# Kernel tuning notes

Measured on AMD Instinct MI355X. Metric: run time of the kernel, lower is better.

The kernel has to match this reference:

```python
import jax, jax.numpy as jnp
from jax import lax
import numpy as np


def _gru(x, h, w_ih, w_hh, b_ih, b_hh):
    # torch.nn.GRUCell: gates ordered (r, z, n)
    gi = x @ w_ih.T + b_ih
    gh = h @ w_hh.T + b_hh
    ir, iz, inn = jnp.split(gi, 3, axis=-1)
    hr, hz, hn = jnp.split(gh, 3, axis=-1)
    r = jax.nn.sigmoid(ir + hr)
    z = jax.nn.sigmoid(iz + hz)
    n = jnp.tanh(inn + r * hn)
    return (1.0 - z) * n + z * h


def _conv(x, w, pad):
    return lax.conv_general_dilated(x, w, (1, 1), [(pad, pad), (pad, pad)],
                                    dimension_numbers=('NCHW', 'OIHW', 'NCHW'))


def _bn(x, g, b):
    # BatchNorm2d in training mode: batch stats over (N,H,W)
    mu = x.mean((0, 2, 3), keepdims=True)
    var = x.var((0, 2, 3), keepdims=True)
    return (x - mu) * lax.rsqrt(var + 1e-5) * g[None, :, None, None] + b[None, :, None, None]


def _forward(features, heights, proj_wtm, mask_outliers, map_height, map_width,
             w_ih, w_hh, b_ih, b_hh,
             c1_w, bn1_g, bn1_b, c2_w, bn2_g, bn2_b, c3_w, bn3_g, bn3_b,
             c4_w, bn4_g, bn4_b, c5_w, c5_b):
    T, C, H, W = features.shape
    M = map_height * map_width
    P = H * W
    mem_dim = w_hh.shape[1]
    # flat map indices per pixel per frame: map_width*y + x
    idx_all = (map_width * proj_wtm[..., 1] + proj_wtm[..., 0]).astype(jnp.int32).reshape(T, P)
    inliers = ~mask_outliers
    mh_all = jnp.where(inliers, heights + 1000.0, -jnp.inf).reshape(T, P)
    feats_flat = features.reshape(T, C, P)
    pix = jnp.arange(P, dtype=jnp.int32)

    def step(carry, frame):
        state, observed, hmap = carry
        feat, idx, mh = frame  # feat [C,P], idx [P] int, mh [P]
        new_hmap = hmap.at[idx].max(mh)                      # persistent scatter_max
        # winner pixel per map cell: a pixel that attains the new max this frame
        cand = jnp.where(mh == new_hmap[idx], pix, -1)
        winner = jnp.full((M,), -1, dtype=jnp.int32).at[idx].max(cand)
        updated = new_hmap > hmap                            # cells where this frame set a new max
        x = feat.T[jnp.maximum(winner, 0)]                   # [M, C] gathered features
        new_state = _gru(x, state, w_ih, w_hh, b_ih, b_hh)
        state = jnp.where(updated[:, None], new_state, state)
        return (state, observed | updated, new_hmap), None

    init = (jnp.zeros((M, mem_dim), features.dtype),
            jnp.zeros((M,), dtype=bool),
            jnp.zeros((M,), features.dtype))
    (state, observed, hmap), _ = lax.scan(step, init, (feats_flat, idx_all, mh_all))

    memory = state.reshape(map_height, map_width, mem_dim).transpose(2, 0, 1)[None]  # [1,D,mh,mw]
    x = jax.nn.relu(_bn(_conv(memory, c1_w, 3), bn1_g, bn1_b))
    x = jax.nn.relu(_bn(_conv(x, c2_w, 1), bn2_g, bn2_b))
    x = jax.nn.relu(_bn(_conv(x, c3_w, 1), bn3_g, bn3_b))
    x = jax.nn.relu(_bn(_conv(x, c4_w, 1), bn4_g, bn4_b))
    sem = _conv(x, c5_w, 0) + c5_b[None, :, None, None]
    return (sem[0],
            observed.reshape(map_height, map_width),
            hmap.reshape(map_height, map_width))


def setup_inputs() -> dict:
    key = jax.random.key(0)
    ks = jax.random.split(key, 24)
    T, C, H, W = 10, 64, 480, 640
    MH, MW, D, NC = 250, 250, 256, 20
    s = 0.02
    return {
        'features': jax.random.normal(ks[0], (T, C, H, W), jnp.float32),
        'proj_wtm': jax.random.randint(ks[1], (T, H, W, 2), 0, 250, jnp.int32),
        'mask_outliers': jax.random.bernoulli(ks[2], 0.3, (T, H, W)),
        'heights': jax.random.normal(ks[3], (T, H, W), jnp.float32),
        'map_height': MH,
        'map_width': MW,
        'w_ih': jax.random.uniform(ks[4], (3 * D, C), jnp.float32, -0.01, 0.01),
        'w_hh': jax.random.uniform(ks[5], (3 * D, D), jnp.float32, -0.01, 0.01),
        'b_ih': jax.random.uniform(ks[6], (3 * D,), jnp.float32, -0.01, 0.01),
        'b_hh': jnp.zeros((3 * D,), jnp.float32),
        'c1_w': jax.random.normal(ks[7], (128, D, 7, 7), jnp.float32) * s,
        'bn1_g': jnp.ones((128,), jnp.float32), 'bn1_b': jnp.full((128,), 1e-4, jnp.float32),
        'c2_w': jax.random.normal(ks[8], (64, 128, 3, 3), jnp.float32) * s,
        'bn2_g': jnp.ones((64,), jnp.float32), 'bn2_b': jnp.full((64,), 1e-4, jnp.float32),
        'c3_w': jax.random.normal(ks[9], (48, 64, 3, 3), jnp.float32) * s,
        'bn3_g': jnp.ones((48,), jnp.float32), 'bn3_b': jnp.full((48,), 1e-4, jnp.float32),
        'c4_w': jax.random.normal(ks[10], (48, 48, 3, 3), jnp.float32) * s,
        'bn4_g': jnp.ones((48,), jnp.float32), 'bn4_b': jnp.full((48,), 1e-4, jnp.float32),
        'c5_w': jax.random.normal(ks[11], (NC, 48, 1, 1), jnp.float32) * s,
        'c5_b': jnp.zeros((NC,), jnp.float32),
    }


def reference(features, proj_wtm, mask_outliers, heights, map_height, map_width,
              w_ih, w_hh, b_ih, b_hh,
              c1_w, bn1_g, bn1_b, c2_w, bn2_g, bn2_b, c3_w, bn3_g, bn3_b,
              c4_w, bn4_g, bn4_b, c5_w, c5_b):
    return _forward(features, heights, proj_wtm, mask_outliers, map_height, map_width,
                    w_ih, w_hh, b_ih, b_hh,
                    c1_w, bn1_g, bn1_b, c2_w, bn2_g, bn2_b, c3_w, bn3_g, bn3_b,
                    c4_w, bn4_g, bn4_b, c5_w, c5_b)
```

## Files before the change

kernel.cpp:

```cpp
#include <hip/hip_runtime.h>
#include <math.h>

#define T_FRAMES 10
#define C_FEAT   64
#define IMG_H    480
#define IMG_W    640
#define P_PIX    (IMG_H*IMG_W)
#define MAP_H    250
#define MAP_W    250
#define M_CELLS  (MAP_H*MAP_W)
#define D_MEM    256
#define N_CLS    20
#define NPAD     62528

#define PW  272
#define PH  262
#define PP  (PH*PW)

typedef __attribute__((ext_vector_type(8))) short s16x8;
typedef __attribute__((ext_vector_type(4))) float f32x4;

__device__ __forceinline__ unsigned short f2bf(float f) {
    unsigned int u = __float_as_uint(f);
    u += 0x7fffu + ((u >> 16) & 1u);
    return (unsigned short)(u >> 16);
}
__device__ __forceinline__ float bf2f(unsigned short b) {
    return __uint_as_float(((unsigned int)b) << 16);
}
__device__ __forceinline__ uint4 pack8u(float4 a, float4 b) {
    uint4 r;
    r.x = (unsigned int)f2bf(a.x) | ((unsigned int)f2bf(a.y) << 16);
    r.y = (unsigned int)f2bf(a.z) | ((unsigned int)f2bf(a.w) << 16);
    r.z = (unsigned int)f2bf(b.x) | ((unsigned int)f2bf(b.y) << 16);
    r.w = (unsigned int)f2bf(b.z) | ((unsigned int)f2bf(b.w) << 16);
    return r;
}


__global__ __launch_bounds__(256) void k_scatter_all(const int2* __restrict__ proj,
                                                     const int* __restrict__ mask,
                                                     const float* __restrict__ heights,
                                                     unsigned long long* __restrict__ packed,
                                                     int* __restrict__ ps) {
    int t = blockIdx.y;
    int p = blockIdx.x * 256 + threadIdx.x;
    size_t gp = (size_t)t * P_PIX + p;
    ps[gp] = -1;
    if (mask[gp]) return;
    int2 pr = proj[gp];
    int idx = MAP_W * pr.y + pr.x;
    float mh = heights[gp] + 1000.0f;
    unsigned long long pk = ((unsigned long long)__float_as_uint(mh) << 32)
                            | (unsigned int)p;
    atomicMax(packed + (size_t)t * M_CELLS + idx, pk);
}


__global__ __launch_bounds__(256) void k_sched(const unsigned long long* __restrict__ packed,
                                               int* __restrict__ updlist,
                                               int* __restrict__ ps,
                                               int* __restrict__ count,
                                               float* __restrict__ out) {
    int m = blockIdx.x * 256 + threadIdx.x;
    if (m >= M_CELLS) return;
    unsigned int pv = 0;
    bool any = false;
    #pragma unroll
    for (int t = 0; t < T_FRAMES; ++t) {
        unsigned long long pk = packed[(size_t)t * M_CELLS + m];
        unsigned int hb = (unsigned int)(pk >> 32);
        if (hb > pv) {
            int slot = atomicAdd(count + t, 1);
            updlist[t * NPAD + slot] = m;
            ps[(size_t)t * P_PIX + (pk & 0xffffffffu)] = slot;
            pv = hb;
            any = true;
        }
    }
    out[(size_t)N_CLS * M_CELLS + m] = any ? 1.0f : 0.0f;
    out[(size_t)N_CLS * M_CELLS + M_CELLS + m] = __uint_as_float(pv);
}


__global__ __launch_bounds__(256) void k_gx_all(const float* __restrict__ feat_all,
                                                const int* __restrict__ ps,
                                                short* __restrict__ Agx) {
    int t = blockIdx.y;
    int p = blockIdx.x * 256 + threadIdx.x;
    int i = ps[(size_t)t * P_PIX + p];
    if (i < 0) return;
    const float* feat = feat_all + (size_t)t * C_FEAT * P_PIX;
    short* dst = Agx + ((size_t)t * NPAD + i) * 64;
    #pragma unroll
    for (int c8 = 0; c8 < 8; ++c8) {
        unsigned int pk[4];
        #pragma unroll
        for (int q = 0; q < 4; ++q) {
            float f0 = feat[(size_t)(c8 * 8 + 2 * q)     * P_PIX + p];
            float f1 = feat[(size_t)(c8 * 8 + 2 * q + 1) * P_PIX + p];
            pk[q] = (unsigned int)f2bf(f0) | ((unsigned int)f2bf(f1) << 16);
        }
        *(uint4*)(dst + c8 * 8) = make_uint4(pk[0], pk[1], pk[2], pk[3]);
    }
}


__device__ __forceinline__ void wprep_gru_item(int idx,
        const float* __restrict__ w_ih, const float* __restrict__ w_hh,
        short* __restrict__ wq) {
    int gp = idx & 1023, k8 = idx >> 10;
    int tau = gp >> 8, gl = gp & 255;
    unsigned int pk[4];
    #pragma unroll
    for (int q = 0; q < 4; ++q) {
        unsigned int h2[2];
        #pragma unroll
        for (int e = 0; e < 2; ++e) {
            int k = k8 * 8 + q * 2 + e;
            float v = 0.f;
            if (tau == 0)      v = (k < 64) ? w_ih[(size_t)gl * 64 + k]
                                            : w_hh[(size_t)gl * 256 + (k - 64)];
            else if (tau == 1) v = (k < 64) ? w_ih[(size_t)(256 + gl) * 64 + k]
                                            : w_hh[(size_t)(256 + gl) * 256 + (k - 64)];
            else if (tau == 2) v = (k < 64) ? w_ih[(size_t)(512 + gl) * 64 + k] : 0.f;
            else               v = (k < 64) ? 0.f
                                            : w_hh[(size_t)(512 + gl) * 256 + (k - 64)];
            h2[e] = f2bf(v);
        }
        pk[q] = h2[0] | (h2[1] << 16);
    }
    *(uint4*)(wq + (size_t)idx * 8) = make_uint4(pk[0], pk[1], pk[2], pk[3]);
}

__device__ __forceinline__ void wprep_conv_item(int idx, const float* __restrict__ w,
        short* __restrict__ wm, int OC, int CIN, int OCP, int CINP, int KS) {
    int oc  = idx % OCP;
    int t2  = idx / OCP;
    int ci8 = t2 % (CINP / 8);
    int tap = t2 / (CINP / 8);
    unsigned int pk[4];
    #pragma unroll
    for (int q = 0; q < 4; ++q) {
        unsigned int h[2];
        #pragma unroll
        for (int e = 0; e < 2; ++e) {
            int ci = ci8 * 8 + 2*q + e;
            float v = (oc < OC && ci < CIN)
                ? w[((size_t)oc * CIN + ci) * KS * KS + tap] : 0.f;
            h[e] = f2bf(v);
        }
        pk[q] = h[0] | (h[1] << 16);
    }
    *(uint4*)(wm + (size_t)idx * 8) = make_uint4(pk[0], pk[1], pk[2], pk[3]);
}

__global__ __launch_bounds__(256) void k_wprep_all(
        const float* __restrict__ w_ih, const float* __restrict__ w_hh,
        short* __restrict__ wq,
        const float* __restrict__ c1_w, short* __restrict__ wm1,
        const float* __restrict__ c2_w, short* __restrict__ wm2,
        const float* __restrict__ c3_w, short* __restrict__ wm3,
        const float* __restrict__ c4_w, short* __restrict__ wm4) {
    int idx = blockIdx.x * 256 + threadIdx.x;
    switch (blockIdx.y) {
    case 0: if (idx < 40 * 1024)    wprep_gru_item(idx, w_ih, w_hh, wq); break;
    case 1: if (idx < 49*32*128)    wprep_conv_item(idx, c1_w, wm1, 128, 256, 128, 256, 7); break;
    case 2: if (idx < 9*16*64)      wprep_conv_item(idx, c2_w, wm2,  64, 128,  64, 128, 3); break;
    case 3: if (idx < 9*8*64)       wprep_conv_item(idx, c3_w, wm3,  48,  64,  64,  64, 3); break;
    default: if (idx < 9*8*64)      wprep_conv_item(idx, c4_w, wm4,  48,  48,  64,  64, 3); break;
    }
}


__global__ __launch_bounds__(256) void k_grumm4(
        const short* __restrict__ Agx_t,
        const short* __restrict__ wq,
        const float* __restrict__ b_ih, const float* __restrict__ b_hh,
        const int* __restrict__ updlist_t, const int* __restrict__ count_t,
        float* __restrict__ state) {
    int n = *count_t;
    int base = blockIdx.x * 64;
    if (base >= n) return;

    __shared__ alignas(16) char B[64 * 640];
    __shared__ int ml[64];
    const int tid = threadIdx.x;
    if (tid < 64) {
        int i = base + tid; if (i > n - 1) i = n - 1;
        ml[tid] = updlist_t[i];
    }
    __syncthreads();

    for (int e = tid; e < 512; e += 256) {
        int cell = e >> 3, kc = e & 7;
        uint4 v = *(const uint4*)(Agx_t + ((size_t)(base + cell)) * 64 + kc * 8);
        int dst = (cell * 640 + kc * 16) ^ ((cell & 7) << 4);
        *(uint4*)(B + dst) = v;
    }
    for (int e = tid; e < 2048; e += 256) {
        int cell = e >> 5, kc = e & 31;
        const float* sp = state + (size_t)ml[cell] * D_MEM + kc * 8;
        float4 v0 = *(const float4*)sp;
        float4 v1 = *(const float4*)(sp + 4);
        int dst = (cell * 640 + 128 + kc * 16) ^ ((cell & 7) << 4);
        *(uint4*)(B + dst) = pack8u(v0, v1);
    }
    __syncthreads();

    const int w = tid >> 6, l = tid & 63, u = l & 15, s = l >> 4;

    #pragma unroll 1
    for (int g16 = w; g16 < 16; g16 += 4) {
        f32x4 aR[4], aZ[4], aI[4], aH[4];
        #pragma unroll
        for (int cf = 0; cf < 4; ++cf) {
            aR[cf] = (f32x4){0.f,0.f,0.f,0.f}; aZ[cf] = (f32x4){0.f,0.f,0.f,0.f};
            aI[cf] = (f32x4){0.f,0.f,0.f,0.f}; aH[cf] = (f32x4){0.f,0.f,0.f,0.f};
        }

        #pragma unroll
        for (int ck = 0; ck < 10; ++ck) {
            s16x8 b[4];
            #pragma unroll
            for (int cf = 0; cf < 4; ++cf) {
                int cell = 16 * cf + u;
                int byte = (cell * 640 + ck * 64 + s * 16) ^ ((cell & 7) << 4);
                b[cf] = *(const s16x8*)(B + byte);
            }
            const short* wr = wq + ((size_t)(ck * 4 + s) * 1024 + g16 * 16 + u) * 8;
            s16x8 ar = *(const s16x8*)(wr);
            s16x8 az = *(const s16x8*)(wr + 256 * 8);
            s16x8 an = *(const s16x8*)(wr + (ck < 2 ? 512 : 768) * 8);
            #pragma unroll
            for (int cf = 0; cf < 4; ++cf) {
                aR[cf] = __builtin_amdgcn_mfma_f32_16x16x32_bf16(ar, b[cf], aR[cf], 0, 0, 0);
                aZ[cf] = __builtin_amdgcn_mfma_f32_16x16x32_bf16(az, b[cf], aZ[cf], 0, 0, 0);
                if (ck < 2)
                    aI[cf] = __builtin_amdgcn_mfma_f32_16x16x32_bf16(an, b[cf], aI[cf], 0, 0, 0);
                else
                    aH[cf] = __builtin_amdgcn_mfma_f32_16x16x32_bf16(an, b[cf], aH[cf], 0, 0, 0);
            }
        }

        const int d0 = g16 * 16 + 4 * s;
        float bi0[4], bh0[4], bi1[4], bh1[4], bi2[4], bh2[4];
        #pragma unroll
        for (int r = 0; r < 4; ++r) {
            int d = d0 + r;
            bi0[r] = b_ih[d];        bh0[r] = b_hh[d];
            bi1[r] = b_ih[256 + d];  bh1[r] = b_hh[256 + d];
            bi2[r] = b_ih[512 + d];  bh2[r] = b_hh[512 + d];
        }
        #pragma unroll
        for (int cf = 0; cf < 4; ++cf) {
            if (base + 16 * cf + u < n) {
                float* sp = state + (size_t)ml[16 * cf + u] * D_MEM;
                float4 h = *(const float4*)(sp + d0);
                float hv[4] = {h.x, h.y, h.z, h.w};
                float ov[4];
                #pragma unroll
                for (int r = 0; r < 4; ++r) {
                    float rr = aR[cf][r] + bi0[r] + bh0[r];
                    float zz = aZ[cf][r] + bi1[r] + bh1[r];
                    float ii = aI[cf][r] + bi2[r];
                    float hh = aH[cf][r] + bh2[r];
                    float rv = 1.f / (1.f + expf(-rr));
                    float zv = 1.f / (1.f + expf(-zz));
                    float nv = tanhf(ii + rv * hh);
                    ov[r] = (1.f - zv) * nv + zv * hv[r];
                }
                *(float4*)(sp + d0) = make_float4(ov[0], ov[1], ov[2], ov[3]);
            }
        }
    }
}


template<int CINP, int KS, int TLY, bool NORM, bool STATS, bool F32OUT, bool F32IN>
__global__ __launch_bounds__(256) void k_cmfma(const void* __restrict__ in,
                                               const short* __restrict__ wm,
                                               int OCT,
                                               void* __restrict__ out,
                                               int OCS,
                                               const float* __restrict__ sums_in,
                                               const float* __restrict__ sums2_in,
                                               const float* __restrict__ g_in,
                                               const float* __restrict__ b_in,
                                               int OCPREV,
                                               float* __restrict__ sums_out,
                                               float* __restrict__ sums2_out) {
    constexpr int PAD = KS / 2;
    constexpr int BH  = 4 * TLY;
    constexpr int PTW_X = 16 + KS - 1;
    constexpr int PTW_Y = BH + KS - 1;
    __shared__ alignas(16) char patch[PTW_Y * PTW_X * 64];
    __shared__ float scl[NORM ? CINP : 1], shf[NORM ? CINP : 1];
    __shared__ float st1[4][64], st2[4][64];

    const int tid = threadIdx.x;
    const int w   = tid >> 6;
    const int l   = tid & 63;
    const int u   = l & 15;
    const int s   = l >> 4;

    const int x0  = 3 + 16 * blockIdx.x;
    const int y0  = 3 + BH * blockIdx.y;
    const int oc0 = 64 * blockIdx.z;

    if constexpr (NORM) {
        for (int c = tid; c < CINP; c += 256) {
            float sc = 0.f, sh = 0.f;
            if (c < OCPREV) {
                float mu  = sums_in[c] * (1.f / M_CELLS);
                float var = sums2_in[c] * (1.f / M_CELLS) - mu * mu;
                float rs  = rsqrtf(var + 1e-5f);
                sc = g_in[c] * rs;
                sh = b_in[c] - mu * rs * g_in[c];
            }
            scl[c] = sc; shf[c] = sh;
        }
    }

    f32x4 acc[TLY][4];
    #pragma unroll
    for (int yy = 0; yy < TLY; ++yy)
        #pragma unroll
        for (int o = 0; o < 4; ++o)
            acc[yy][o] = (f32x4){0.f, 0.f, 0.f, 0.f};

    for (int ci0 = 0; ci0 < CINP; ci0 += 32) {
        __syncthreads();
        for (int e = tid; e < PTW_Y * PTW_X * 4; e += 256) {
            int c8 = e & 3;
            int pp = e >> 2;
            int px = pp % PTW_X, py = pp / PTW_X;
            int gy = y0 - PAD + py, gx = x0 - PAD + px;
            bool inb = (gy >= 3) && (gy < 253) && (gx >= 3) && (gx < 253);
            uint4 v = make_uint4(0, 0, 0, 0);
            if constexpr (F32IN) {
                if (inb) {
                    int m = (gy - 3) * MAP_W + (gx - 3);
                    const float* sp = (const float*)in + (size_t)m * 256 + ci0 + c8 * 8;
                    float4 v0 = *(const float4*)sp;
                    float4 v1 = *(const float4*)(sp + 4);
                    v = pack8u(v0, v1);
                }
            } else {
                v = *(const uint4*)((const short*)in + ((size_t)gy * PW + gx) * CINP
                                    + ci0 + c8 * 8);
                if constexpr (NORM) {
                    int cb = ci0 + c8 * 8;
                    unsigned int uu[4] = {v.x, v.y, v.z, v.w};
                    unsigned int ro[4];
                    #pragma unroll
                    for (int q = 0; q < 4; ++q) {
                        float f0 = bf2f((unsigned short)(uu[q] & 0xffffu));
                        float f1 = bf2f((unsigned short)(uu[q] >> 16));
                        f0 = fmaxf(fmaf(f0, scl[cb + 2*q],     shf[cb + 2*q]),     0.f);
                        f1 = fmaxf(fmaf(f1, scl[cb + 2*q + 1], shf[cb + 2*q + 1]), 0.f);
                        ro[q] = (unsigned int)f2bf(f0) | ((unsigned int)f2bf(f1) << 16);
                    }
                    v = make_uint4(ro[0], ro[1], ro[2], ro[3]);
                }
                if (!inb) v = make_uint4(0, 0, 0, 0);
            }
            int lb = (((py * PTW_X + px) * 64) + c8 * 16) ^ ((px & 3) << 4);
            *(uint4*)(patch + lb) = v;
        }
        __syncthreads();

        const short* wb = wm + ((size_t)(ci0 / 8 + s) * OCT + oc0 + u) * 8;

        for (int ky = 0; ky < KS; ++ky) {
            for (int kx = 0; kx < KS; ++kx) {
                const int tap = ky * KS + kx;
                const short* wt = wb + (size_t)tap * (CINP / 8) * OCT * 8;
                s16x8 a[4];
                #pragma unroll
                for (int o = 0; o < 4; ++o)
                    a[o] = *(const s16x8*)(wt + o * 16 * 8);
                const int px = kx + u;
                const int lb0 = ((px * 64) + s * 16) ^ ((px & 3) << 4);
                #pragma unroll
                for (int yy = 0; yy < TLY; ++yy) {
                    int py = TLY * w + yy + ky;
                    s16x8 b = *(const s16x8*)(patch + py * PTW_X * 64 + lb0);
                    #pragma unroll
                    for (int o = 0; o < 4; ++o)
                        acc[yy][o] = __builtin_amdgcn_mfma_f32_16x16x32_bf16(
                            a[o], b, acc[yy][o], 0, 0, 0);
                }
            }
        }
    }

    const int gx = x0 + u;
    const bool colok = (gx < 253);

    if constexpr (STATS) {
        float s1[16], s2[16];
        #pragma unroll
        for (int e = 0; e < 16; ++e) { s1[e] = 0.f; s2[e] = 0.f; }
        #pragma unroll
        for (int yy = 0; yy < TLY; ++yy) {
            int gy = y0 + TLY * w + yy;
            if (colok && gy < 253) {
                #pragma unroll
                for (int o = 0; o < 4; ++o)
                    #pragma unroll
                    for (int r = 0; r < 4; ++r) {
                        float v = acc[yy][o][r];
                        s1[o*4+r] += v; s2[o*4+r] += v * v;
                    }
            }
        }
        #pragma unroll
        for (int off = 1; off < 16; off <<= 1)
            #pragma unroll
            for (int e = 0; e < 16; ++e) {
                s1[e] += __shfl_xor(s1[e], off, 64);
                s2[e] += __shfl_xor(s2[e], off, 64);
            }
        if (u == 0) {
            #pragma unroll
            for (int e = 0; e < 16; ++e) {
                int ch = (e >> 2) * 16 + s * 4 + (e & 3);
                st1[w][ch] = s1[e]; st2[w][ch] = s2[e];
            }
        }
        __syncthreads();
        if (tid < 64) {
            float a1 = st1[0][tid] + st1[1][tid] + st1[2][tid] + st1[3][tid];
            float a2 = st2[0][tid] + st2[1][tid] + st2[2][tid] + st2[3][tid];
            atomicAdd(sums_out  + oc0 + tid, a1);
            atomicAdd(sums2_out + oc0 + tid, a2);
        }
    }

    if (!colok) return;
    #pragma unroll
    for (int yy = 0; yy < TLY; ++yy) {
        int gy = y0 + TLY * w + yy;
        if (gy >= 253) continue;
        #pragma unroll
        for (int o = 0; o < 4; ++o) {
            int oc = oc0 + o * 16 + s * 4;
            if constexpr (F32OUT) {
                int m = (gy - 3) * MAP_W + (gx - 3);
                float* op = (float*)out + (size_t)m * 48 + oc;
                #pragma unroll
                for (int r = 0; r < 4; ++r)
                    if (oc + r < 48) op[r] = acc[yy][o][r];
            } else {
                short* op = (short*)out + ((size_t)gy * PW + gx) * OCS + oc;
                unsigned int w0 = f2bf(acc[yy][o][0]) | ((unsigned int)f2bf(acc[yy][o][1]) << 16);
                unsigned int w1 = f2bf(acc[yy][o][2]) | ((unsigned int)f2bf(acc[yy][o][3]) << 16);
                *(uint2*)op = make_uint2(w0, w1);
            }
        }
    }
}


__global__ __launch_bounds__(256) void k_conv5(const float* __restrict__ x4,
                                               const float* __restrict__ w,
                                               const float* __restrict__ bias,
                                               const float* __restrict__ sums4,
                                               const float* __restrict__ sums24,
                                               const float* __restrict__ g4,
                                               const float* __restrict__ b4,
                                               float* __restrict__ sem) {
    __shared__ float wl[N_CLS * 48];
    __shared__ float scl[48], shf[48], bl[N_CLS];
    int tid = threadIdx.x;
    for (int e = tid; e < N_CLS * 48; e += 256) wl[e] = w[e];
    if (tid < 48) {
        float mu  = sums4[tid] * (1.f / M_CELLS);
        float var = sums24[tid] * (1.f / M_CELLS) - mu * mu;
        float rs  = rsqrtf(var + 1e-5f);
        scl[tid] = g4[tid] * rs;
        shf[tid] = b4[tid] - mu * rs * g4[tid];
    }
    if (tid < N_CLS) bl[tid] = bias[tid];
    __syncthreads();
    int p = blockIdx.x * 256 + tid;
    if (p >= M_CELLS) return;
    float inr[48];
    const float4* xp = (const float4*)(x4 + (size_t)p * 48);
    #pragma unroll
    for (int q = 0; q < 12; ++q) {
        float4 v = xp[q];
        inr[4*q+0] = v.x; inr[4*q+1] = v.y; inr[4*q+2] = v.z; inr[4*q+3] = v.w;
    }
    #pragma unroll
    for (int c = 0; c < 48; ++c)
        inr[c] = fmaxf(fmaf(inr[c], scl[c], shf[c]), 0.f);
    #pragma unroll
    for (int o = 0; o < N_CLS; ++o) {
        float a = bl[o];
        #pragma unroll
        for (int c = 0; c < 48; ++c) a = fmaf(inr[c], wl[o * 48 + c], a);
        sem[(size_t)o * M_CELLS + p] = a;
    }
}


extern "C" void kernel_launch(void* const* d_in, const int* in_sizes, int n_in,
                              void* d_out, int out_size, void* d_ws, size_t ws_size,
                              hipStream_t stream) {
    (void)in_sizes; (void)n_in; (void)out_size; (void)ws_size;

    const float* features = (const float*)d_in[0];
    const int*   proj     = (const int*)d_in[1];
    const int*   mask     = (const int*)d_in[2];
    const float* heights  = (const float*)d_in[3];
    const float* w_ih  = (const float*)d_in[6];
    const float* w_hh  = (const float*)d_in[7];
    const float* b_ih  = (const float*)d_in[8];
    const float* b_hh  = (const float*)d_in[9];
    const float* c1_w  = (const float*)d_in[10];
    const float* bn1_g = (const float*)d_in[11];
    const float* bn1_b = (const float*)d_in[12];
    const float* c2_w  = (const float*)d_in[13];
    const float* bn2_g = (const float*)d_in[14];
    const float* bn2_b = (const float*)d_in[15];
    const float* c3_w  = (const float*)d_in[16];
    const float* bn3_g = (const float*)d_in[17];
    const float* bn3_b = (const float*)d_in[18];
    const float* c4_w  = (const float*)d_in[19];
    const float* bn4_g = (const float*)d_in[20];
    const float* bn4_b = (const float*)d_in[21];
    const float* c5_w  = (const float*)d_in[22];
    const float* c5_b  = (const float*)d_in[23];

    char* ws = (char*)d_ws;
    float* state = (float*)(ws);
    unsigned long long* packed = (unsigned long long*)(ws + 64000000);
    int*   count   = (int*)(ws + 69000000);
    float* sums    = (float*)(ws + 69000064);
    float* sums2   = (float*)(ws + 69002112);
    int*   ps      = (int*)(ws + 70000000);
    int*   updlist = (int*)(ws + 83000000);
    short* Agx     = (short*)(ws + 86000000);
    short* wq      = (short*)(ws + 167000000);
    short* wm1     = (short*)(ws + 168000000);
    short* wm2     = (short*)(ws + 171300000);
    short* wm3     = (short*)(ws + 171500000);
    short* wm4     = (short*)(ws + 171600000);
    short* x1_cl   = (short*)(ws + 172000000);
    short* x2_cl   = (short*)(ws + 191000000);
    short* x3_cl   = (short*)(ws + 201000000);
    float* x4      = (float*)(ws + 211000000);

    hipMemsetAsync(ws, 0, 69004160, stream);

    k_wprep_all<<<dim3(784, 5), 256, 0, stream>>>(w_ih, w_hh, wq,
                                                  c1_w, wm1, c2_w, wm2,
                                                  c3_w, wm3, c4_w, wm4);

    const int PB = P_PIX / 256;
    const int MB = (M_CELLS + 255) / 256;
    const int CB = NPAD / 64;

    k_scatter_all<<<dim3(PB, T_FRAMES), 256, 0, stream>>>(
        (const int2*)proj, mask, heights, packed, ps);
    k_sched<<<MB, 256, 0, stream>>>(packed, updlist, ps, count, (float*)d_out);
    k_gx_all<<<dim3(PB, T_FRAMES), 256, 0, stream>>>(features, ps, Agx);

    for (int t = 0; t < T_FRAMES; ++t) {
        k_grumm4<<<CB, 256, 0, stream>>>(Agx + (size_t)t * NPAD * 64, wq,
                                         b_ih, b_hh,
                                         updlist + t * NPAD, count + t, state);
    }

    k_cmfma<256, 7, 8, false, true, false, true><<<dim3(16, 8, 2), 256, 0, stream>>>(
        state, wm1, 128, x1_cl, 128,
        nullptr, nullptr, nullptr, nullptr, 0, sums + 0, sums2 + 0);

    k_cmfma<128, 3, 4, true, true, false, false><<<dim3(16, 16, 1), 256, 0, stream>>>(
        x1_cl, wm2, 64, x2_cl, 64,
        sums + 0, sums2 + 0, bn1_g, bn1_b, 128, sums + 128, sums2 + 128);

    k_cmfma<64, 3, 4, true, true, false, false><<<dim3(16, 16, 1), 256, 0, stream>>>(
        x2_cl, wm3, 64, x3_cl, 64,
        sums + 128, sums2 + 128, bn2_g, bn2_b, 64, sums + 192, sums2 + 192);

    k_cmfma<64, 3, 4, true, true, true, false><<<dim3(16, 16, 1), 256, 0, stream>>>(
        x3_cl, wm4, 64, x4, 48,
        sums + 192, sums2 + 192, bn3_g, bn3_b, 48, sums + 256, sums2 + 256);

    k_conv5<<<MB, 256, 0, stream>>>(x4, c5_w, c5_b,
                                    sums + 256, sums2 + 256, bn4_g, bn4_b,
                                    (float*)d_out);
}
```

Baseline: 1.297 ms.

## Fuse per-frame GRU launches into one persistent kernel with grid barrier

Replaces the ten per-frame GRU kernel launches with one persistent kernel of 768 blocks. The blocks loop over frames and cell tiles and meet at a spin-wait global barrier on atomic counters between frames. This removes launch overhead and the idle tails between frames, at the cost of barrier spin time and a deadlock risk if the 768 blocks are not all resident at once (launch bounds ask for 3 blocks per CU). It also splits the MFMA k-loop to remove a branch and moves the bias loads inline. The conv1 tile height is halved and its grid doubled.

```diff
diff --git a/kernel.cpp b/kernel.cpp
--- a/kernel.cpp
+++ b/kernel.cpp
@@ -12,6 +12,7 @@
 #define D_MEM    256
 #define N_CLS    20
 #define NPAD     62528
+#define GBLK2    768
 
 #define PW  272
 #define PH  262
@@ -173,106 +174,130 @@
 }
 
 
-__global__ __launch_bounds__(256) void k_grumm4(
-        const short* __restrict__ Agx_t,
+__global__ __launch_bounds__(256, 3) void k_gruchain2(
+        const short* __restrict__ Agx,
         const short* __restrict__ wq,
         const float* __restrict__ b_ih, const float* __restrict__ b_hh,
-        const int* __restrict__ updlist_t, const int* __restrict__ count_t,
-        float* __restrict__ state) {
-    int n = *count_t;
-    int base = blockIdx.x * 64;
-    if (base >= n) return;
-
+        const int* __restrict__ updlist, const int* __restrict__ count,
+        float* __restrict__ state, int* __restrict__ bar) {
     __shared__ alignas(16) char B[64 * 640];
     __shared__ int ml[64];
     const int tid = threadIdx.x;
-    if (tid < 64) {
-        int i = base + tid; if (i > n - 1) i = n - 1;
-        ml[tid] = updlist_t[i];
-    }
-    __syncthreads();
-
-    for (int e = tid; e < 512; e += 256) {
-        int cell = e >> 3, kc = e & 7;
-        uint4 v = *(const uint4*)(Agx_t + ((size_t)(base + cell)) * 64 + kc * 8);
-        int dst = (cell * 640 + kc * 16) ^ ((cell & 7) << 4);
-        *(uint4*)(B + dst) = v;
-    }
-    for (int e = tid; e < 2048; e += 256) {
-        int cell = e >> 5, kc = e & 31;
-        const float* sp = state + (size_t)ml[cell] * D_MEM + kc * 8;
-        float4 v0 = *(const float4*)sp;
-        float4 v1 = *(const float4*)(sp + 4);
-        int dst = (cell * 640 + 128 + kc * 16) ^ ((cell & 7) << 4);
-        *(uint4*)(B + dst) = pack8u(v0, v1);
-    }
-    __syncthreads();
-
     const int w = tid >> 6, l = tid & 63, u = l & 15, s = l >> 4;
 
-    #pragma unroll 1
-    for (int g16 = w; g16 < 16; g16 += 4) {
-        f32x4 aR[4], aZ[4], aI[4], aH[4];
-        #pragma unroll
-        for (int cf = 0; cf < 4; ++cf) {
-            aR[cf] = (f32x4){0.f,0.f,0.f,0.f}; aZ[cf] = (f32x4){0.f,0.f,0.f,0.f};
-            aI[cf] = (f32x4){0.f,0.f,0.f,0.f}; aH[cf] = (f32x4){0.f,0.f,0.f,0.f};
-        }
-
-        #pragma unroll
-        for (int ck = 0; ck < 10; ++ck) {
-            s16x8 b[4];
-            #pragma unroll
-            for (int cf = 0; cf < 4; ++cf) {
-                int cell = 16 * cf + u;
-                int byte = (cell * 640 + ck * 64 + s * 16) ^ ((cell & 7) << 4);
-                b[cf] = *(const s16x8*)(B + byte);
-            }
-            const short* wr = wq + ((size_t)(ck * 4 + s) * 1024 + g16 * 16 + u) * 8;
-            s16x8 ar = *(const s16x8*)(wr);
-            s16x8 az = *(const s16x8*)(wr + 256 * 8);
-            s16x8 an = *(const s16x8*)(wr + (ck < 2 ? 512 : 768) * 8);
-            #pragma unroll
-            for (int cf = 0; cf < 4; ++cf) {
-                aR[cf] = __builtin_amdgcn_mfma_f32_16x16x32_bf16(ar, b[cf], aR[cf], 0, 0, 0);
-                aZ[cf] = __builtin_amdgcn_mfma_f32_16x16x32_bf16(az, b[cf], aZ[cf], 0, 0, 0);
-                if (ck < 2)
-                    aI[cf] = __builtin_amdgcn_mfma_f32_16x16x32_bf16(an, b[cf], aI[cf], 0, 0, 0);
-                else
-                    aH[cf] = __builtin_amdgcn_mfma_f32_16x16x32_bf16(an, b[cf], aH[cf], 0, 0, 0);
-            }
-        }
-
-        const int d0 = g16 * 16 + 4 * s;
-        float bi0[4], bh0[4], bi1[4], bh1[4], bi2[4], bh2[4];
-        #pragma unroll
-        for (int r = 0; r < 4; ++r) {
-            int d = d0 + r;
-            bi0[r] = b_ih[d];        bh0[r] = b_hh[d];
-            bi1[r] = b_ih[256 + d];  bh1[r] = b_hh[256 + d];
-            bi2[r] = b_ih[512 + d];  bh2[r] = b_hh[512 + d];
-        }
-        #pragma unroll
-        for (int cf = 0; cf < 4; ++cf) {
-            if (base + 16 * cf + u < n) {
-                float* sp = state + (size_t)ml[16 * cf + u] * D_MEM;
-                float4 h = *(const float4*)(sp + d0);
-                float hv[4] = {h.x, h.y, h.z, h.w};
-                float ov[4];
+    for (int t = 0; t < T_FRAMES; ++t) {
+        const int n = count[t];
+        const short* Agx_t = Agx + (size_t)t * NPAD * 64;
+        const int* upd = updlist + t * NPAD;
+
+        for (int base = blockIdx.x * 64; base < n; base += GBLK2 * 64) {
+            __syncthreads();
+            if (tid < 64) {
+                int i = base + tid; if (i > n - 1) i = n - 1;
+                ml[tid] = upd[i];
+            }
+            __syncthreads();
+
+            for (int e = tid; e < 512; e += 256) {
+                int cell = e >> 3, kc = e & 7;
+                uint4 v = *(const uint4*)(Agx_t + ((size_t)(base + cell)) * 64 + kc * 8);
+                int dst = (cell * 640 + kc * 16) ^ ((cell & 7) << 4);
+                *(uint4*)(B + dst) = v;
+            }
+            for (int e = tid; e < 2048; e += 256) {
+                int cell = e >> 5, kc = e & 31;
+                const float* sp = state + (size_t)ml[cell] * D_MEM + kc * 8;
+                float4 v0 = *(const float4*)sp;
+                float4 v1 = *(const float4*)(sp + 4);
+                int dst = (cell * 640 + 128 + kc * 16) ^ ((cell & 7) << 4);
+                *(uint4*)(B + dst) = pack8u(v0, v1);
+            }
+            __syncthreads();
+
+            #pragma unroll 1
+            for (int g16 = w; g16 < 16; g16 += 4) {
+                f32x4 aR[4], aZ[4], aI[4], aH[4];
                 #pragma unroll
-                for (int r = 0; r < 4; ++r) {
-                    float rr = aR[cf][r] + bi0[r] + bh0[r];
-                    float zz = aZ[cf][r] + bi1[r] + bh1[r];
-                    float ii = aI[cf][r] + bi2[r];
-                    float hh = aH[cf][r] + bh2[r];
-                    float rv = 1.f / (1.f + expf(-rr));
-                    float zv = 1.f / (1.f + expf(-zz));
-                    float nv = tanhf(ii + rv * hh);
-                    ov[r] = (1.f - zv) * nv + zv * hv[r];
+                for (int cf = 0; cf < 4; ++cf) {
+                    aR[cf] = (f32x4){0.f,0.f,0.f,0.f}; aZ[cf] = (f32x4){0.f,0.f,0.f,0.f};
+                    aI[cf] = (f32x4){0.f,0.f,0.f,0.f}; aH[cf] = (f32x4){0.f,0.f,0.f,0.f};
                 }
-                *(float4*)(sp + d0) = make_float4(ov[0], ov[1], ov[2], ov[3]);
-            }
-        }
+
+                #pragma unroll
+                for (int ck = 0; ck < 2; ++ck) {
+                    s16x8 b[4];
+                    #pragma unroll
+                    for (int cf = 0; cf < 4; ++cf) {
+                        int cell = 16 * cf + u;
+                        int byte = (cell * 640 + ck * 64 + s * 16) ^ ((cell & 7) << 4);
+                        b[cf] = *(const s16x8*)(B + byte);
+                    }
+                    const short* wr = wq + ((size_t)(ck * 4 + s) * 1024 + g16 * 16 + u) * 8;
+                    s16x8 ar = *(const s16x8*)(wr);
+                    s16x8 az = *(const s16x8*)(wr + 256 * 8);
+                    s16x8 an = *(const s16x8*)(wr + 512 * 8);
+                    #pragma unroll
+                    for (int cf = 0; cf < 4; ++cf) {
+                        aR[cf] = __builtin_amdgcn_mfma_f32_16x16x32_bf16(ar, b[cf], aR[cf], 0, 0, 0);
+                        aZ[cf] = __builtin_amdgcn_mfma_f32_16x16x32_bf16(az, b[cf], aZ[cf], 0, 0, 0);
+                        aI[cf] = __builtin_amdgcn_mfma_f32_16x16x32_bf16(an, b[cf], aI[cf], 0, 0, 0);
+                    }
+                }
+                #pragma unroll 2
+                for (int ck = 2; ck < 10; ++ck) {
+                    s16x8 b[4];
+                    #pragma unroll
+                    for (int cf = 0; cf < 4; ++cf) {
+                        int cell = 16 * cf + u;
+                        int byte = (cell * 640 + ck * 64 + s * 16) ^ ((cell & 7) << 4);
+                        b[cf] = *(const s16x8*)(B + byte);
+                    }
+                    const short* wr = wq + ((size_t)(ck * 4 + s) * 1024 + g16 * 16 + u) * 8;
+                    s16x8 ar = *(const s16x8*)(wr);
+                    s16x8 az = *(const s16x8*)(wr + 256 * 8);
+                    s16x8 an = *(const s16x8*)(wr + 768 * 8);
+                    #pragma unroll
+                    for (int cf = 0; cf < 4; ++cf) {
+                        aR[cf] = __builtin_amdgcn_mfma_f32_16x16x32_bf16(ar, b[cf], aR[cf], 0, 0, 0);
+                        aZ[cf] = __builtin_amdgcn_mfma_f32_16x16x32_bf16(az, b[cf], aZ[cf], 0, 0, 0);
+                        aH[cf] = __builtin_amdgcn_mfma_f32_16x16x32_bf16(an, b[cf], aH[cf], 0, 0, 0);
+                    }
+                }
+
+                const int d0 = g16 * 16 + 4 * s;
+                #pragma unroll
+                for (int cf = 0; cf < 4; ++cf) {
+                    if (base + 16 * cf + u < n) {
+                        float* sp = state + (size_t)ml[16 * cf + u] * D_MEM;
+                        float4 h = *(const float4*)(sp + d0);
+                        float hv[4] = {h.x, h.y, h.z, h.w};
+                        float ov[4];
+                        #pragma unroll
+                        for (int r = 0; r < 4; ++r) {
+                            int d = d0 + r;
+                            float rr = aR[cf][r] + b_ih[d]       + b_hh[d];
+                            float zz = aZ[cf][r] + b_ih[256 + d] + b_hh[256 + d];
+                            float ii = aI[cf][r] + b_ih[512 + d];
+                            float hh = aH[cf][r] + b_hh[512 + d];
+                            float rv = 1.f / (1.f + expf(-rr));
+                            float zv = 1.f / (1.f + expf(-zz));
+                            float nv = tanhf(ii + rv * hh);
+                            ov[r] = (1.f - zv) * nv + zv * hv[r];
+                        }
+                        *(float4*)(sp + d0) = make_float4(ov[0], ov[1], ov[2], ov[3]);
+                    }
+                }
+            }
+        }
+
+        __syncthreads();
+        __threadfence();
+        if (tid == 0) {
+            atomicAdd(bar + t, 1);
+            while (atomicAdd(bar + t, 0) < GBLK2) __builtin_amdgcn_s_sleep(8);
+        }
+        __syncthreads();
+        __threadfence();
     }
 }
 
@@ -540,6 +565,7 @@
     int*   count   = (int*)(ws + 69000000);
     float* sums    = (float*)(ws + 69000064);
     float* sums2   = (float*)(ws + 69002112);
+    int*   bar     = (int*)(ws + 69004160);
     int*   ps      = (int*)(ws + 70000000);
     int*   updlist = (int*)(ws + 83000000);
     short* Agx     = (short*)(ws + 86000000);
@@ -553,7 +579,7 @@
     short* x3_cl   = (short*)(ws + 201000000);
     float* x4      = (float*)(ws + 211000000);
 
-    hipMemsetAsync(ws, 0, 69004160, stream);
+    hipMemsetAsync(ws, 0, 69004224, stream);
 
     k_wprep_all<<<dim3(784, 5), 256, 0, stream>>>(w_ih, w_hh, wq,
                                                   c1_w, wm1, c2_w, wm2,
@@ -561,20 +587,16 @@
 
     const int PB = P_PIX / 256;
     const int MB = (M_CELLS + 255) / 256;
-    const int CB = NPAD / 64;
 
     k_scatter_all<<<dim3(PB, T_FRAMES), 256, 0, stream>>>(
         (const int2*)proj, mask, heights, packed, ps);
     k_sched<<<MB, 256, 0, stream>>>(packed, updlist, ps, count, (float*)d_out);
     k_gx_all<<<dim3(PB, T_FRAMES), 256, 0, stream>>>(features, ps, Agx);
 
-    for (int t = 0; t < T_FRAMES; ++t) {
-        k_grumm4<<<CB, 256, 0, stream>>>(Agx + (size_t)t * NPAD * 64, wq,
-                                         b_ih, b_hh,
-                                         updlist + t * NPAD, count + t, state);
-    }
-
-    k_cmfma<256, 7, 8, false, true, false, true><<<dim3(16, 8, 2), 256, 0, stream>>>(
+    k_gruchain2<<<GBLK2, 256, 0, stream>>>(Agx, wq, b_ih, b_hh,
+                                           updlist, count, state, bar);
+
+    k_cmfma<256, 7, 4, false, true, false, true><<<dim3(16, 16, 2), 256, 0, stream>>>(
         state, wm1, 128, x1_cl, 128,
         nullptr, nullptr, nullptr, nullptr, 0, sums + 0, sums2 + 0);
 
```

New measurement: 2.586 ms. 1.99x slower.
